# Performance work log

Measured on AMD Instinct MI355X. Metric: run time of the kernel, lower is better.

The kernel has to match this reference:

```python
import jax, jax.numpy as jnp
import numpy as np

HEAD_SIZE = 64  # hidden_size / num_attention_heads = 1024 / 16


def setup_inputs() -> dict:
    key = jax.random.key(0)
    k1, k2, k3, k4, k5 = jax.random.split(key, 5)
    B, S, H, R = 4, 2048, 1024, 1
    hidden_states = jax.random.normal(k1, (B, S, H), dtype=jnp.float32)
    attention_mask = jnp.zeros((B, S), dtype=jnp.float32)  # additive mask
    value_w = jax.random.normal(k2, (H, H), dtype=jnp.float32) * (1.0 / np.sqrt(H))
    value_b = jax.random.normal(k3, (H,), dtype=jnp.float32) * 0.02
    U = jax.random.normal(k4, (H + 1, R), dtype=jnp.float32)
    V = jax.random.normal(k5, (R, H + 1), dtype=jnp.float32)
    return {"hidden_states": hidden_states, "attention_mask": attention_mask,
            "value_w": value_w, "value_b": value_b, "U": U, "V": V}


def reference(hidden_states, attention_mask, value_w, value_b, U, V):
    B, S, H = hidden_states.shape
    # value projection (nn.Linear applies x @ W^T + b)
    value_layer = hidden_states @ value_w.T + value_b  # [B,S,H]
    # X = [hidden_states, 1] -> [B,S,H+1]
    ones = jnp.ones((B, S, 1), dtype=hidden_states.dtype)
    X = jnp.concatenate([hidden_states, ones], axis=-1)
    # scores = X (U V) X^T, computed via the low-rank factorization:
    # (X U) [B,S,R] @ (X V^T)^T [B,R,S] -- mathematically identical, avoids
    # materializing the (H+1)x(H+1) matrix M.
    XU = X @ U            # [B,S,R]
    XVt = X @ V.T         # [B,S,R]
    scores = jnp.einsum('bsr,btr->bst', XU, XVt) / jnp.sqrt(jnp.float32(HEAD_SIZE))
    # additive attention mask, broadcast as [B,1,S]
    scores = scores + attention_mask[:, None, :]
    probs = jax.nn.softmax(scores, axis=-1)  # [B,S,S]
    # dropout p=0.0 (eval) -> identity
    context = jnp.einsum('bst,bth->bsh', probs, value_layer)  # [B,S,H]
    return context
```

## Files before the change

kernel.cpp:

```cpp
#include <hip/hip_runtime.h>
#include <hip/hip_bf16.h>
#include <stdint.h>

#define LOG2E 1.44269504088896340736f

typedef float f32x4 __attribute__((ext_vector_type(4)));
typedef __bf16 bf16x8 __attribute__((ext_vector_type(8)));

__device__ __forceinline__ void g2lds16(const void* g, void* l) {
  __builtin_amdgcn_global_load_lds(
      (__attribute__((address_space(1))) unsigned int*)g,
      (__attribute__((address_space(3))) unsigned int*)l,
      16, 0, 0);
}

__device__ __forceinline__ unsigned short f2bf_u(float f) {
  __bf16 h = (__bf16)f;
  return __builtin_bit_cast(unsigned short, h);
}

__global__ void __launch_bounds__(256) fused_prep(
    const float* __restrict__ hidden, const float* __restrict__ U,
    const float* __restrict__ V, const float* __restrict__ vw,
    unsigned short* __restrict__ hbf, unsigned short* __restrict__ wbf,
    float* __restrict__ aL, float* __restrict__ vArr) {
  int tid = threadIdx.x;
  int pid = blockIdx.x;
  if (pid < 512) {
    int lane = tid & 63, w = tid >> 6;
    int xcd = pid & 7, idx = pid >> 3;
    int row0 = (xcd << 10) + (idx * 4 + w) * 4;
    float4 u4[4], v4[4];
#pragma unroll
    for (int c = 0; c < 4; ++c) {
      u4[c] = *(const float4*)&U[c * 256 + lane * 4];
      v4[c] = *(const float4*)&V[c * 256 + lane * 4];
    }
    float u_t = U[1024], v_t = V[1024];
    float su[4], sv[4];
#pragma unroll
    for (int r = 0; r < 4; ++r) {
      const float* hr = hidden + (size_t)(row0 + r) * 1024;
      unsigned short* hb = hbf + (size_t)(row0 + r) * 1024;
      float ssu = 0.f, ssv = 0.f;
#pragma unroll
      for (int c = 0; c < 4; ++c) {
        float4 x = *(const float4*)&hr[c * 256 + lane * 4];
        ushort4 o;
        o.x = f2bf_u(x.x); o.y = f2bf_u(x.y); o.z = f2bf_u(x.z); o.w = f2bf_u(x.w);
        *(ushort4*)&hb[c * 256 + lane * 4] = o;
        ssu += x.x * u4[c].x + x.y * u4[c].y + x.z * u4[c].z + x.w * u4[c].w;
        ssv += x.x * v4[c].x + x.y * v4[c].y + x.z * v4[c].z + x.w * v4[c].w;
      }
      su[r] = ssu; sv[r] = ssv;
    }
#pragma unroll
    for (int off = 1; off < 64; off <<= 1) {
#pragma unroll
      for (int r = 0; r < 4; ++r) {
        su[r] += __shfl_xor(su[r], off);
        sv[r] += __shfl_xor(sv[r], off);
      }
    }
    if (lane < 4) {
      int r = lane;
      float sur = (r == 0) ? su[0] : (r == 1) ? su[1] : (r == 2) ? su[2] : su[3];
      float svr = (r == 0) ? sv[0] : (r == 1) ? sv[1] : (r == 2) ? sv[2] : sv[3];
      aL[row0 + r] = (sur + u_t) * 0.125f * LOG2E;
      vArr[row0 + r] = svr + v_t;
    }
  } else {
    int wp = pid - 512;
#pragma unroll
    for (int it = 0; it < 8; ++it) {
      int idx = (wp * 256 + tid) * 4 + it * 131072;
      float4 x = *(const float4*)&vw[idx];
      ushort4 o;
      o.x = f2bf_u(x.x); o.y = f2bf_u(x.y); o.z = f2bf_u(x.z); o.w = f2bf_u(x.w);
      *(ushort4*)&wbf[idx] = o;
    }
  }
}

__global__ void __launch_bounds__(256) gemm_stats(
    const unsigned short* __restrict__ hbf, const unsigned short* __restrict__ wbf,
    const float* __restrict__ bias, unsigned short* __restrict__ vlt,
    const float* __restrict__ aL, const float* __restrict__ vArr,
    const float* __restrict__ mask, unsigned short* __restrict__ P,
    int statsBlocks) {
  __shared__ __align__(16) char sA[128 * 256];
  __shared__ __align__(16) char sB[128 * 256];
  int tid = threadIdx.x;
  int pid = blockIdx.x;
  if (pid >= statsBlocks) {
    int g = pid - statsBlocks;
    int lane = tid & 63, wave = tid >> 6;
    int xcd = g & 7, kk = g >> 3;
    int m0 = (xcd * 8 + (kk >> 3)) * 128;
    int n0 = (kk & 7) * 128;
    int rl = lane >> 4, pc = lane & 15;
    int wr = wave >> 1, wc = wave & 1;
    int m_ = lane & 15, q = lane >> 4;
    f32x4 acc[4][4] = {};
    for (int k0 = 0; k0 < 1024; k0 += 128) {
      __syncthreads();
#pragma unroll
      for (int ii = 0; ii < 8; ++ii) {
        int rb = wave * 32 + ii * 4;
        int r = rb + rl;
        int gc = pc ^ (r & 15);
        g2lds16(hbf + (size_t)(m0 + r) * 1024 + k0 + gc * 8, sA + rb * 256);
        g2lds16(wbf + (size_t)(n0 + r) * 1024 + k0 + gc * 8, sB + rb * 256);
      }
      __syncthreads();
#pragma unroll
      for (int ks = 0; ks < 4; ++ks) {
        bf16x8 af[4], bfr[4];
#pragma unroll
        for (int i = 0; i < 4; ++i)
          af[i] = *(const bf16x8*)(sA + (wr * 64 + i * 16 + m_) * 256 + (((ks * 4 + q) ^ m_) * 16));
#pragma unroll
        for (int j = 0; j < 4; ++j)
          bfr[j] = *(const bf16x8*)(sB + (wc * 64 + j * 16 + m_) * 256 + (((ks * 4 + q) ^ m_) * 16));
#pragma unroll
        for (int i = 0; i < 4; ++i)
#pragma unroll
          for (int j = 0; j < 4; ++j)
            acc[i][j] = __builtin_amdgcn_mfma_f32_16x16x32_bf16(af[i], bfr[j], acc[i][j], 0, 0, 0);
      }
    }
#pragma unroll
    for (int jt = 0; jt < 4; ++jt) {
      int j = n0 + wc * 64 + jt * 16 + m_;
      float bj = bias[j];
#pragma unroll
      for (int it = 0; it < 4; ++it) {
        int i = m0 + wr * 64 + it * 16 + q * 4;
        f32x4 a = acc[it][jt];
        ushort4 o;
        o.x = f2bf_u(a.x + bj); o.y = f2bf_u(a.y + bj);
        o.z = f2bf_u(a.z + bj); o.w = f2bf_u(a.w + bj);
        *(ushort4*)&vlt[(size_t)j * 8192 + i] = o;
      }
    }
  } else {
    int b = pid;
    int lane = tid & 63, w = tid >> 6;
    int xcd = b & 7, idx = b >> 3;
    int row0 = (xcd << 10) + (idx * 4 + w) * 8;
    int tb = (row0 >> 11) << 11;
    float4 va[8], ma[8];
#pragma unroll
    for (int c = 0; c < 4; ++c) {
      int t = c * 512 + lane * 8;
      va[2 * c]     = *(const float4*)&vArr[tb + t];
      va[2 * c + 1] = *(const float4*)&vArr[tb + t + 4];
      float4 m0v = *(const float4*)&mask[tb + t];
      float4 m1v = *(const float4*)&mask[tb + t + 4];
      ma[2 * c].x = m0v.x * LOG2E; ma[2 * c].y = m0v.y * LOG2E;
      ma[2 * c].z = m0v.z * LOG2E; ma[2 * c].w = m0v.w * LOG2E;
      ma[2 * c + 1].x = m1v.x * LOG2E; ma[2 * c + 1].y = m1v.y * LOG2E;
      ma[2 * c + 1].z = m1v.z * LOG2E; ma[2 * c + 1].w = m1v.w * LOG2E;
    }
#pragma unroll
    for (int r = 0; r < 8; ++r) {
      int row = row0 + r;
      float a = aL[row];
      float s[32];
#pragma unroll
      for (int qq = 0; qq < 8; ++qq) {
        s[qq * 4 + 0] = fmaf(a, va[qq].x, ma[qq].x);
        s[qq * 4 + 1] = fmaf(a, va[qq].y, ma[qq].y);
        s[qq * 4 + 2] = fmaf(a, va[qq].z, ma[qq].z);
        s[qq * 4 + 3] = fmaf(a, va[qq].w, ma[qq].w);
      }
      float mx = s[0];
#pragma unroll
      for (int u = 1; u < 32; ++u) mx = fmaxf(mx, s[u]);
#pragma unroll
      for (int off = 1; off < 64; off <<= 1) mx = fmaxf(mx, __shfl_xor(mx, off));
      float z = 0.f;
#pragma unroll
      for (int u = 0; u < 32; ++u) {
        s[u] = __builtin_amdgcn_exp2f(s[u] - mx);
        z += s[u];
      }
#pragma unroll
      for (int off = 1; off < 64; off <<= 1) z += __shfl_xor(z, off);
      float iz = __builtin_amdgcn_rcpf(z);
      unsigned short* pr = P + (size_t)row * 2048;
#pragma unroll
      for (int c = 0; c < 4; ++c) {
        bf16x8 o;
#pragma unroll
        for (int u = 0; u < 8; ++u) o[u] = (__bf16)(iz * s[c * 8 + u]);
        *(bf16x8*)&pr[c * 512 + lane * 8] = o;
      }
    }
  }
}

__global__ void __launch_bounds__(256) attn(
    const unsigned short* __restrict__ p, const unsigned short* __restrict__ vlt,
    float* __restrict__ out) {
  __shared__ __align__(16) char sA[128 * 256];
  __shared__ __align__(16) char sB[128 * 256];
  int tid = threadIdx.x;
  int lane = tid & 63, wave = tid >> 6;
  int pid = blockIdx.x;
  int xcd = pid & 7, kk = pid >> 3;
  int i0 = (xcd * 8 + (kk >> 3)) * 128;
  int h0 = (kk & 7) * 128;
  int b = i0 >> 11;
  size_t toff = (size_t)b << 11;
  int rl = lane >> 4, pc = lane & 15;
  int wr = wave >> 1, wc = wave & 1;
  int m_ = lane & 15, q = lane >> 4;
  f32x4 acc[4][4] = {};
  for (int k0 = 0; k0 < 2048; k0 += 128) {
    __syncthreads();
#pragma unroll
    for (int ii = 0; ii < 8; ++ii) {
      int rb = wave * 32 + ii * 4;
      int r = rb + rl;
      int gc = pc ^ (r & 15);
      g2lds16(p + (size_t)(i0 + r) * 2048 + k0 + gc * 8, sA + rb * 256);
      g2lds16(vlt + (size_t)(h0 + r) * 8192 + toff + k0 + gc * 8, sB + rb * 256);
    }
    __syncthreads();
#pragma unroll
    for (int ks = 0; ks < 4; ++ks) {
      bf16x8 af[4], bfr[4];
#pragma unroll
      for (int i = 0; i < 4; ++i)
        af[i] = *(const bf16x8*)(sA + (wr * 64 + i * 16 + m_) * 256 + (((ks * 4 + q) ^ m_) * 16));
#pragma unroll
      for (int j = 0; j < 4; ++j)
        bfr[j] = *(const bf16x8*)(sB + (wc * 64 + j * 16 + m_) * 256 + (((ks * 4 + q) ^ m_) * 16));
#pragma unroll
      for (int i = 0; i < 4; ++i)
#pragma unroll
        for (int j = 0; j < 4; ++j)
          acc[i][j] = __builtin_amdgcn_mfma_f32_16x16x32_bf16(af[i], bfr[j], acc[i][j], 0, 0, 0);
    }
  }
#pragma unroll
  for (int it = 0; it < 4; ++it) {
    int gi = i0 + wr * 64 + it * 16 + q * 4;
#pragma unroll
    for (int jt = 0; jt < 4; ++jt) {
      int h = h0 + wc * 64 + jt * 16 + m_;
      f32x4 a = acc[it][jt];
      out[(size_t)(gi + 0) * 1024 + h] = a.x;
      out[(size_t)(gi + 1) * 1024 + h] = a.y;
      out[(size_t)(gi + 2) * 1024 + h] = a.z;
      out[(size_t)(gi + 3) * 1024 + h] = a.w;
    }
  }
}

extern "C" void kernel_launch(void* const* d_in, const int* in_sizes, int n_in,
                              void* d_out, int out_size, void* d_ws, size_t ws_size,
                              hipStream_t stream) {
  const float* hidden = (const float*)d_in[0];
  const float* mask   = (const float*)d_in[1];
  const float* vw     = (const float*)d_in[2];
  const float* vb     = (const float*)d_in[3];
  const float* U      = (const float*)d_in[4];
  const float* V      = (const float*)d_in[5];
  float* out = (float*)d_out;
  char* ws = (char*)d_ws;

  if (ws_size >= 69271552ull) {
    unsigned short* hbf = (unsigned short*)ws;
    unsigned short* wbf = (unsigned short*)(ws + 16777216);
    unsigned short* vlt = (unsigned short*)(ws + 18874368);
    unsigned short* P   = (unsigned short*)(ws + 35651584);
    float* aL   = (float*)(ws + 69206016);
    float* vArr = aL + 8192;
    fused_prep<<<640, 256, 0, stream>>>(hidden, U, V, vw, hbf, wbf, aL, vArr);
    gemm_stats<<<768, 256, 0, stream>>>(hbf, wbf, vb, vlt, aL, vArr, mask, P, 256);
    attn<<<512, 256, 0, stream>>>(P, vlt, out);
  } else {
    unsigned short* hbf = (unsigned short*)ws;
    unsigned short* wbf = (unsigned short*)(ws + 16777216);
    unsigned short* P   = (unsigned short*)ws;
    unsigned short* vlt = (unsigned short*)(ws + 33554432);
    float* aL   = (float*)(ws + 50331648);
    float* vArr = aL + 8192;
    fused_prep<<<640, 256, 0, stream>>>(hidden, U, V, vw, hbf, wbf, aL, vArr);
    gemm_stats<<<512, 256, 0, stream>>>(hbf, wbf, vb, vlt, aL, vArr, mask, P, 0);
    gemm_stats<<<256, 256, 0, stream>>>(hbf, wbf, vb, vlt, aL, vArr, mask, P, 256);
    attn<<<512, 256, 0, stream>>>(P, vlt, out);
  }
}
```

Baseline: 157.7 us.

## Merge stats, value GEMM and attention into persistent kernel with flag-based dependencies

Replaces the separate gemm_stats and attn launches with one persistent kernel. Blocks pull work items from an atomic counter: softmax-probability rows first, then value-projection tiles, then attention output tiles. Each attention tile waits on a completion counter for P and on per-tile flags for the value tiles it needs. This removes a kernel-boundary drain and lets attention tiles start while late projection tiles finish. It adds spin-wait synchronisation, a control array reset in the prep kernel, and a risk of deadlock or stalls if dependency ordering or occupancy assumptions break.

After: 549.8 us. 3.49x slower.

```diff
diff --git a/kernel.cpp b/kernel.cpp
--- a/kernel.cpp
+++ b/kernel.cpp
@@ -23,9 +23,13 @@
     const float* __restrict__ hidden, const float* __restrict__ U,
     const float* __restrict__ V, const float* __restrict__ vw,
     unsigned short* __restrict__ hbf, unsigned short* __restrict__ wbf,
-    float* __restrict__ aL, float* __restrict__ vArr) {
+    float* __restrict__ aL, float* __restrict__ vArr,
+    unsigned int* __restrict__ ctrl) {
   int tid = threadIdx.x;
   int pid = blockIdx.x;
+  if (ctrl != nullptr && pid == 0) {
+    for (int i = tid; i < 544; i += 256) ctrl[i] = 0u;
+  }
   if (pid < 512) {
     int lane = tid & 63, w = tid >> 6;
     int xcd = pid & 7, idx = pid >> 3;
@@ -78,6 +82,203 @@
       ushort4 o;
       o.x = f2bf_u(x.x); o.y = f2bf_u(x.y); o.z = f2bf_u(x.z); o.w = f2bf_u(x.w);
       *(ushort4*)&wbf[idx] = o;
+    }
+  }
+}
+
+__global__ void __launch_bounds__(256) mega(
+    const unsigned short* __restrict__ hbf, const unsigned short* __restrict__ wbf,
+    const float* __restrict__ bias, unsigned short* __restrict__ vlt,
+    const float* __restrict__ aL, const float* __restrict__ vArr,
+    const float* __restrict__ mask, unsigned short* __restrict__ P,
+    float* __restrict__ out, unsigned int* __restrict__ ctrl) {
+  __shared__ __align__(16) char sA[128 * 256];
+  __shared__ __align__(16) char sB[128 * 256];
+  __shared__ unsigned int s_t;
+  unsigned int* flags = ctrl + 16;
+  int tid = threadIdx.x;
+  for (;;) {
+    __syncthreads();
+    if (tid == 0) s_t = atomicAdd(&ctrl[0], 1u);
+    __syncthreads();
+    unsigned int t = s_t;
+    if (t >= 1280u) return;
+    if (t < 256u) {
+      int lane = tid & 63, w = tid >> 6;
+      int row0 = (int)t * 32 + w * 8;
+      int tb = (row0 >> 11) << 11;
+      float4 va[8], ma[8];
+#pragma unroll
+      for (int c = 0; c < 4; ++c) {
+        int tt = c * 512 + lane * 8;
+        va[2 * c]     = *(const float4*)&vArr[tb + tt];
+        va[2 * c + 1] = *(const float4*)&vArr[tb + tt + 4];
+        float4 m0v = *(const float4*)&mask[tb + tt];
+        float4 m1v = *(const float4*)&mask[tb + tt + 4];
+        ma[2 * c].x = m0v.x * LOG2E; ma[2 * c].y = m0v.y * LOG2E;
+        ma[2 * c].z = m0v.z * LOG2E; ma[2 * c].w = m0v.w * LOG2E;
+        ma[2 * c + 1].x = m1v.x * LOG2E; ma[2 * c + 1].y = m1v.y * LOG2E;
+        ma[2 * c + 1].z = m1v.z * LOG2E; ma[2 * c + 1].w = m1v.w * LOG2E;
+      }
+#pragma unroll
+      for (int r = 0; r < 8; ++r) {
+        int row = row0 + r;
+        float a = aL[row];
+        float s[32];
+#pragma unroll
+        for (int qq = 0; qq < 8; ++qq) {
+          s[qq * 4 + 0] = fmaf(a, va[qq].x, ma[qq].x);
+          s[qq * 4 + 1] = fmaf(a, va[qq].y, ma[qq].y);
+          s[qq * 4 + 2] = fmaf(a, va[qq].z, ma[qq].z);
+          s[qq * 4 + 3] = fmaf(a, va[qq].w, ma[qq].w);
+        }
+        float mx = s[0];
+#pragma unroll
+        for (int u = 1; u < 32; ++u) mx = fmaxf(mx, s[u]);
+#pragma unroll
+        for (int off = 1; off < 64; off <<= 1) mx = fmaxf(mx, __shfl_xor(mx, off));
+        float z = 0.f;
+#pragma unroll
+        for (int u = 0; u < 32; ++u) {
+          s[u] = __builtin_amdgcn_exp2f(s[u] - mx);
+          z += s[u];
+        }
+#pragma unroll
+        for (int off = 1; off < 64; off <<= 1) z += __shfl_xor(z, off);
+        float iz = __builtin_amdgcn_rcpf(z);
+        unsigned short* pr = P + (size_t)row * 2048;
+#pragma unroll
+        for (int c = 0; c < 4; ++c) {
+          bf16x8 o;
+#pragma unroll
+          for (int u = 0; u < 8; ++u) o[u] = (__bf16)(iz * s[c * 8 + u]);
+          *(bf16x8*)&pr[c * 512 + lane * 8] = o;
+        }
+      }
+      __syncthreads();
+      if (tid == 0) {
+        __threadfence();
+        __hip_atomic_fetch_add(&ctrl[1], 1u, __ATOMIC_RELEASE, __HIP_MEMORY_SCOPE_AGENT);
+      }
+    } else if (t < 768u) {
+      unsigned int fq = t - 256u;
+      int m0 = (int)(fq & 63u) * 128;
+      int n0 = (int)(fq >> 6) * 128;
+      int lane = tid & 63, wave = tid >> 6;
+      int rl = lane >> 4, pc = lane & 15;
+      int wr = wave >> 1, wc = wave & 1;
+      int m_ = lane & 15, qq = lane >> 4;
+      f32x4 acc[4][4] = {};
+      for (int k0 = 0; k0 < 1024; k0 += 128) {
+        __syncthreads();
+#pragma unroll
+        for (int ii = 0; ii < 8; ++ii) {
+          int rb = wave * 32 + ii * 4;
+          int r = rb + rl;
+          int gc = pc ^ (r & 15);
+          g2lds16(hbf + (size_t)(m0 + r) * 1024 + k0 + gc * 8, sA + rb * 256);
+          g2lds16(wbf + (size_t)(n0 + r) * 1024 + k0 + gc * 8, sB + rb * 256);
+        }
+        __syncthreads();
+#pragma unroll
+        for (int ks = 0; ks < 4; ++ks) {
+          bf16x8 af[4], bfr[4];
+#pragma unroll
+          for (int i = 0; i < 4; ++i)
+            af[i] = *(const bf16x8*)(sA + (wr * 64 + i * 16 + m_) * 256 + (((ks * 4 + qq) ^ m_) * 16));
+#pragma unroll
+          for (int j = 0; j < 4; ++j)
+            bfr[j] = *(const bf16x8*)(sB + (wc * 64 + j * 16 + m_) * 256 + (((ks * 4 + qq) ^ m_) * 16));
+#pragma unroll
+          for (int i = 0; i < 4; ++i)
+#pragma unroll
+            for (int j = 0; j < 4; ++j)
+              acc[i][j] = __builtin_amdgcn_mfma_f32_16x16x32_bf16(af[i], bfr[j], acc[i][j], 0, 0, 0);
+        }
+      }
+#pragma unroll
+      for (int jt = 0; jt < 4; ++jt) {
+        int j = n0 + wc * 64 + jt * 16 + m_;
+        float bj = bias[j];
+#pragma unroll
+        for (int it = 0; it < 4; ++it) {
+          int i = m0 + wr * 64 + it * 16 + qq * 4;
+          f32x4 a = acc[it][jt];
+          ushort4 o;
+          o.x = f2bf_u(a.x + bj); o.y = f2bf_u(a.y + bj);
+          o.z = f2bf_u(a.z + bj); o.w = f2bf_u(a.w + bj);
+          *(ushort4*)&vlt[(size_t)j * 8192 + i] = o;
+        }
+      }
+      __syncthreads();
+      if (tid == 0) {
+        __threadfence();
+        __hip_atomic_store(&flags[fq], 1u, __ATOMIC_RELEASE, __HIP_MEMORY_SCOPE_AGENT);
+      }
+    } else {
+      unsigned int at = t - 768u;
+      int N = (int)(at >> 6), I = (int)(at & 63u);
+      int i0 = I * 128, h0 = N * 128;
+      int b = I >> 4;
+      size_t toff = (size_t)b << 11;
+      unsigned int qbase = ((unsigned)N << 6) | ((unsigned)b << 4);
+      int lane = tid & 63, wave = tid >> 6;
+      int rl = lane >> 4, pc = lane & 15;
+      int wr = wave >> 1, wc = wave & 1;
+      int m_ = lane & 15, qq = lane >> 4;
+      if (tid == 0) {
+        while (__hip_atomic_load(&ctrl[1], __ATOMIC_ACQUIRE, __HIP_MEMORY_SCOPE_AGENT) < 256u)
+          __builtin_amdgcn_s_sleep(2);
+        __threadfence();
+      }
+      f32x4 acc[4][4] = {};
+      for (int k0 = 0; k0 < 2048; k0 += 128) {
+        __syncthreads();
+        if (tid == 0) {
+          unsigned int fq = qbase + (unsigned)(k0 >> 7);
+          while (__hip_atomic_load(&flags[fq], __ATOMIC_ACQUIRE, __HIP_MEMORY_SCOPE_AGENT) == 0u)
+            __builtin_amdgcn_s_sleep(2);
+          __threadfence();
+        }
+        __syncthreads();
+#pragma unroll
+        for (int ii = 0; ii < 8; ++ii) {
+          int rb = wave * 32 + ii * 4;
+          int r = rb + rl;
+          int gc = pc ^ (r & 15);
+          g2lds16(P + (size_t)(i0 + r) * 2048 + k0 + gc * 8, sA + rb * 256);
+          g2lds16(vlt + (size_t)(h0 + r) * 8192 + toff + k0 + gc * 8, sB + rb * 256);
+        }
+        __syncthreads();
+#pragma unroll
+        for (int ks = 0; ks < 4; ++ks) {
+          bf16x8 af[4], bfr[4];
+#pragma unroll
+          for (int i = 0; i < 4; ++i)
+            af[i] = *(const bf16x8*)(sA + (wr * 64 + i * 16 + m_) * 256 + (((ks * 4 + qq) ^ m_) * 16));
+#pragma unroll
+          for (int j = 0; j < 4; ++j)
+            bfr[j] = *(const bf16x8*)(sB + (wc * 64 + j * 16 + m_) * 256 + (((ks * 4 + qq) ^ m_) * 16));
+#pragma unroll
+          for (int i = 0; i < 4; ++i)
+#pragma unroll
+            for (int j = 0; j < 4; ++j)
+              acc[i][j] = __builtin_amdgcn_mfma_f32_16x16x32_bf16(af[i], bfr[j], acc[i][j], 0, 0, 0);
+        }
+      }
+#pragma unroll
+      for (int it = 0; it < 4; ++it) {
+        int gi = i0 + wr * 64 + it * 16 + qq * 4;
+#pragma unroll
+        for (int jt = 0; jt < 4; ++jt) {
+          int h = h0 + wc * 64 + jt * 16 + m_;
+          f32x4 a = acc[it][jt];
+          out[(size_t)(gi + 0) * 1024 + h] = a.x;
+          out[(size_t)(gi + 1) * 1024 + h] = a.y;
+          out[(size_t)(gi + 2) * 1024 + h] = a.z;
+          out[(size_t)(gi + 3) * 1024 + h] = a.w;
+        }
+      }
     }
   }
 }
@@ -271,16 +472,16 @@
   float* out = (float*)d_out;
   char* ws = (char*)d_ws;
 
-  if (ws_size >= 69271552ull) {
+  if (ws_size >= 69275648ull) {
     unsigned short* hbf = (unsigned short*)ws;
     unsigned short* wbf = (unsigned short*)(ws + 16777216);
     unsigned short* vlt = (unsigned short*)(ws + 18874368);
     unsigned short* P   = (unsigned short*)(ws + 35651584);
     float* aL   = (float*)(ws + 69206016);
     float* vArr = aL + 8192;
-    fused_prep<<<640, 256, 0, stream>>>(hidden, U, V, vw, hbf, wbf, aL, vArr);
-    gemm_stats<<<768, 256, 0, stream>>>(hbf, wbf, vb, vlt, aL, vArr, mask, P, 256);
-    attn<<<512, 256, 0, stream>>>(P, vlt, out);
+    unsigned int* ctrl = (unsigned int*)(ws + 69271552);
+    fused_prep<<<640, 256, 0, stream>>>(hidden, U, V, vw, hbf, wbf, aL, vArr, ctrl);
+    mega<<<512, 256, 0, stream>>>(hbf, wbf, vb, vlt, aL, vArr, mask, P, out, ctrl);
   } else {
     unsigned short* hbf = (unsigned short*)ws;
     unsigned short* wbf = (unsigned short*)(ws + 16777216);
@@ -288,7 +489,7 @@
     unsigned short* vlt = (unsigned short*)(ws + 33554432);
     float* aL   = (float*)(ws + 50331648);
     float* vArr = aL + 8192;
-    fused_prep<<<640, 256, 0, stream>>>(hidden, U, V, vw, hbf, wbf, aL, vArr);
+    fused_prep<<<640, 256, 0, stream>>>(hidden, U, V, vw, hbf, wbf, aL, vArr, nullptr);
     gemm_stats<<<512, 256, 0, stream>>>(hbf, wbf, vb, vlt, aL, vArr, mask, P, 0);
     gemm_stats<<<256, 256, 0, stream>>>(hbf, wbf, vb, vlt, aL, vArr, mask, P, 256);
     attn<<<512, 256, 0, stream>>>(P, vlt, out);
```

## Double-buffer LDS tiles with async prefetch in value GEMM and attention GEMM

Applied to the files above, without the earlier changes.

Both bf16 GEMM loops move from a single 128-wide K tile loaded and then computed under two full syncthreads to two 64-wide K buffers. The next tile is prefetched with global_load_lds while the current one is computed, using an explicit vmcnt wait and raw s_barrier. The goal is to hide global-to-LDS load latency behind MFMA work. In exchange, the K step is halved, doubling the number of barriers, and the swizzle changes to an 8-chunk XOR pattern. The hand-written vmcnt counts depend on the exact number of outstanding loads per thread.

After: 166.1 us. +5.3%, slower.

```diff
diff --git a/kernel.cpp b/kernel.cpp
--- a/kernel.cpp
+++ b/kernel.cpp
@@ -88,8 +88,8 @@
     const float* __restrict__ aL, const float* __restrict__ vArr,
     const float* __restrict__ mask, unsigned short* __restrict__ P,
     int statsBlocks) {
-  __shared__ __align__(16) char sA[128 * 256];
-  __shared__ __align__(16) char sB[128 * 256];
+  __shared__ __align__(16) char sA[2][128 * 128];
+  __shared__ __align__(16) char sB[2][128 * 128];
   int tid = threadIdx.x;
   int pid = blockIdx.x;
   if (pid >= statsBlocks) {
@@ -98,36 +98,55 @@
     int xcd = g & 7, kk = g >> 3;
     int m0 = (xcd * 8 + (kk >> 3)) * 128;
     int n0 = (kk & 7) * 128;
-    int rl = lane >> 4, pc = lane & 15;
+    int r8 = lane >> 3, c8 = lane & 7;
     int wr = wave >> 1, wc = wave & 1;
     int m_ = lane & 15, q = lane >> 4;
+#pragma unroll
+    for (int ii = 0; ii < 4; ++ii) {
+      int rb = wave * 32 + ii * 8;
+      int r = rb + r8;
+      int gc = c8 ^ (r & 7);
+      g2lds16(hbf + (size_t)(m0 + r) * 1024 + gc * 8, sA[0] + rb * 128);
+      g2lds16(wbf + (size_t)(n0 + r) * 1024 + gc * 8, sB[0] + rb * 128);
+    }
     f32x4 acc[4][4] = {};
-    for (int k0 = 0; k0 < 1024; k0 += 128) {
-      __syncthreads();
-#pragma unroll
-      for (int ii = 0; ii < 8; ++ii) {
-        int rb = wave * 32 + ii * 4;
-        int r = rb + rl;
-        int gc = pc ^ (r & 15);
-        g2lds16(hbf + (size_t)(m0 + r) * 1024 + k0 + gc * 8, sA + rb * 256);
-        g2lds16(wbf + (size_t)(n0 + r) * 1024 + k0 + gc * 8, sB + rb * 256);
-      }
-      __syncthreads();
-#pragma unroll
-      for (int ks = 0; ks < 4; ++ks) {
+    for (int k = 0; k < 16; ++k) {
+      int cur = k & 1;
+      if (k < 15) {
+        int k0n = (k + 1) * 64;
+#pragma unroll
+        for (int ii = 0; ii < 4; ++ii) {
+          int rb = wave * 32 + ii * 8;
+          int r = rb + r8;
+          int gc = c8 ^ (r & 7);
+          g2lds16(hbf + (size_t)(m0 + r) * 1024 + k0n + gc * 8, sA[cur ^ 1] + rb * 128);
+          g2lds16(wbf + (size_t)(n0 + r) * 1024 + k0n + gc * 8, sB[cur ^ 1] + rb * 128);
+        }
+        asm volatile("s_waitcnt vmcnt(8)" ::: "memory");
+      } else {
+        asm volatile("s_waitcnt vmcnt(0)" ::: "memory");
+      }
+      __builtin_amdgcn_s_barrier();
+      asm volatile("" ::: "memory");
+      const char* ca = sA[cur];
+      const char* cb = sB[cur];
+#pragma unroll
+      for (int ks = 0; ks < 2; ++ks) {
         bf16x8 af[4], bfr[4];
 #pragma unroll
         for (int i = 0; i < 4; ++i)
-          af[i] = *(const bf16x8*)(sA + (wr * 64 + i * 16 + m_) * 256 + (((ks * 4 + q) ^ m_) * 16));
+          af[i] = *(const bf16x8*)(ca + (wr * 64 + i * 16 + m_) * 128 + (((ks * 4 + q) ^ (m_ & 7)) * 16));
 #pragma unroll
         for (int j = 0; j < 4; ++j)
-          bfr[j] = *(const bf16x8*)(sB + (wc * 64 + j * 16 + m_) * 256 + (((ks * 4 + q) ^ m_) * 16));
+          bfr[j] = *(const bf16x8*)(cb + (wc * 64 + j * 16 + m_) * 128 + (((ks * 4 + q) ^ (m_ & 7)) * 16));
 #pragma unroll
         for (int i = 0; i < 4; ++i)
 #pragma unroll
           for (int j = 0; j < 4; ++j)
             acc[i][j] = __builtin_amdgcn_mfma_f32_16x16x32_bf16(af[i], bfr[j], acc[i][j], 0, 0, 0);
       }
+      asm volatile("" ::: "memory");
+      __builtin_amdgcn_s_barrier();
     }
 #pragma unroll
     for (int jt = 0; jt < 4; ++jt) {
@@ -203,8 +222,8 @@
 __global__ void __launch_bounds__(256) attn(
     const unsigned short* __restrict__ p, const unsigned short* __restrict__ vlt,
     float* __restrict__ out) {
-  __shared__ __align__(16) char sA[128 * 256];
-  __shared__ __align__(16) char sB[128 * 256];
+  __shared__ __align__(16) char sA[2][128 * 128];
+  __shared__ __align__(16) char sB[2][128 * 128];
   int tid = threadIdx.x;
   int lane = tid & 63, wave = tid >> 6;
   int pid = blockIdx.x;
@@ -213,36 +232,55 @@
   int h0 = (kk & 7) * 128;
   int b = i0 >> 11;
   size_t toff = (size_t)b << 11;
-  int rl = lane >> 4, pc = lane & 15;
+  int r8 = lane >> 3, c8 = lane & 7;
   int wr = wave >> 1, wc = wave & 1;
   int m_ = lane & 15, q = lane >> 4;
+#pragma unroll
+  for (int ii = 0; ii < 4; ++ii) {
+    int rb = wave * 32 + ii * 8;
+    int r = rb + r8;
+    int gc = c8 ^ (r & 7);
+    g2lds16(p + (size_t)(i0 + r) * 2048 + gc * 8, sA[0] + rb * 128);
+    g2lds16(vlt + (size_t)(h0 + r) * 8192 + toff + gc * 8, sB[0] + rb * 128);
+  }
   f32x4 acc[4][4] = {};
-  for (int k0 = 0; k0 < 2048; k0 += 128) {
-    __syncthreads();
-#pragma unroll
-    for (int ii = 0; ii < 8; ++ii) {
-      int rb = wave * 32 + ii * 4;
-      int r = rb + rl;
-      int gc = pc ^ (r & 15);
-      g2lds16(p + (size_t)(i0 + r) * 2048 + k0 + gc * 8, sA + rb * 256);
-      g2lds16(vlt + (size_t)(h0 + r) * 8192 + toff + k0 + gc * 8, sB + rb * 256);
-    }
-    __syncthreads();
-#pragma unroll
-    for (int ks = 0; ks < 4; ++ks) {
+  for (int k = 0; k < 32; ++k) {
+    int cur = k & 1;
+    if (k < 31) {
+      int k0n = (k + 1) * 64;
+#pragma unroll
+      for (int ii = 0; ii < 4; ++ii) {
+        int rb = wave * 32 + ii * 8;
+        int r = rb + r8;
+        int gc = c8 ^ (r & 7);
+        g2lds16(p + (size_t)(i0 + r) * 2048 + k0n + gc * 8, sA[cur ^ 1] + rb * 128);
+        g2lds16(vlt + (size_t)(h0 + r) * 8192 + toff + k0n + gc * 8, sB[cur ^ 1] + rb * 128);
+      }
+      asm volatile("s_waitcnt vmcnt(8)" ::: "memory");
+    } else {
+      asm volatile("s_waitcnt vmcnt(0)" ::: "memory");
+    }
+    __builtin_amdgcn_s_barrier();
+    asm volatile("" ::: "memory");
+    const char* ca = sA[cur];
+    const char* cb = sB[cur];
+#pragma unroll
+    for (int ks = 0; ks < 2; ++ks) {
       bf16x8 af[4], bfr[4];
 #pragma unroll
       for (int i = 0; i < 4; ++i)
-        af[i] = *(const bf16x8*)(sA + (wr * 64 + i * 16 + m_) * 256 + (((ks * 4 + q) ^ m_) * 16));
+        af[i] = *(const bf16x8*)(ca + (wr * 64 + i * 16 + m_) * 128 + (((ks * 4 + q) ^ (m_ & 7)) * 16));
 #pragma unroll
       for (int j = 0; j < 4; ++j)
-        bfr[j] = *(const bf16x8*)(sB + (wc * 64 + j * 16 + m_) * 256 + (((ks * 4 + q) ^ m_) * 16));
+        bfr[j] = *(const bf16x8*)(cb + (wc * 64 + j * 16 + m_) * 128 + (((ks * 4 + q) ^ (m_ & 7)) * 16));
 #pragma unroll
       for (int i = 0; i < 4; ++i)
 #pragma unroll
         for (int j = 0; j < 4; ++j)
           acc[i][j] = __builtin_amdgcn_mfma_f32_16x16x32_bf16(af[i], bfr[j], acc[i][j], 0, 0, 0);
     }
+    asm volatile("" ::: "memory");
+    __builtin_amdgcn_s_barrier();
   }
 #pragma unroll
   for (int it = 0; it < 4; ++it) {
```

## Triple-buffer attn PV GEMM with 256x128 tiles and 512-thread blocks

Applied to the files above, without the earlier changes.

Rewrites the final probs×V GEMM kernel to use 256x128 output tiles computed by 8 waves, with a 3-stage LDS ring of 64-wide K slices loaded asynchronously. Explicit vmcnt waits and one barrier per step replace the two-barrier load/compute pattern, and s_setprio is raised around the MFMA blocks. The aim is to overlap global→LDS traffic with MFMA work and to reload the B tile less often. In exchange it uses more LDS (about 144KB) and more accumulator registers per wave, and launches only 256 blocks, which may limit occupancy on the CUs.

Result: slower. 172.4 us (+9.4%).

```diff
diff --git a/kernel.cpp b/kernel.cpp
--- a/kernel.cpp
+++ b/kernel.cpp
@@ -200,57 +200,91 @@
   }
 }
 
-__global__ void __launch_bounds__(256) attn(
-    const unsigned short* __restrict__ p, const unsigned short* __restrict__ vlt,
+__global__ void __launch_bounds__(512, 2) attn(
+    const unsigned short* __restrict__ P, const unsigned short* __restrict__ vlt,
     float* __restrict__ out) {
-  __shared__ __align__(16) char sA[128 * 256];
-  __shared__ __align__(16) char sB[128 * 256];
+  __shared__ __align__(16) char sA[3][256 * 128];
+  __shared__ __align__(16) char sB[3][128 * 128];
   int tid = threadIdx.x;
   int lane = tid & 63, wave = tid >> 6;
   int pid = blockIdx.x;
   int xcd = pid & 7, kk = pid >> 3;
-  int i0 = (xcd * 8 + (kk >> 3)) * 128;
+  int mt = xcd * 4 + (kk >> 3);
+  int i0 = mt * 256;
   int h0 = (kk & 7) * 128;
-  int b = i0 >> 11;
-  size_t toff = (size_t)b << 11;
-  int rl = lane >> 4, pc = lane & 15;
-  int wr = wave >> 1, wc = wave & 1;
+  size_t toff = (size_t)(mt >> 3) << 11;
+  int r8 = lane >> 3, c8 = lane & 7;
+  int wr = wave >> 2, wcn = wave & 3;
   int m_ = lane & 15, q = lane >> 4;
-  f32x4 acc[4][4] = {};
-  for (int k0 = 0; k0 < 2048; k0 += 128) {
-    __syncthreads();
-#pragma unroll
-    for (int ii = 0; ii < 8; ++ii) {
-      int rb = wave * 32 + ii * 4;
-      int r = rb + rl;
-      int gc = pc ^ (r & 15);
-      g2lds16(p + (size_t)(i0 + r) * 2048 + k0 + gc * 8, sA + rb * 256);
-      g2lds16(vlt + (size_t)(h0 + r) * 8192 + toff + k0 + gc * 8, sB + rb * 256);
-    }
-    __syncthreads();
-#pragma unroll
-    for (int ks = 0; ks < 4; ++ks) {
-      bf16x8 af[4], bfr[4];
-#pragma unroll
-      for (int i = 0; i < 4; ++i)
-        af[i] = *(const bf16x8*)(sA + (wr * 64 + i * 16 + m_) * 256 + (((ks * 4 + q) ^ m_) * 16));
-#pragma unroll
-      for (int j = 0; j < 4; ++j)
-        bfr[j] = *(const bf16x8*)(sB + (wc * 64 + j * 16 + m_) * 256 + (((ks * 4 + q) ^ m_) * 16));
-#pragma unroll
-      for (int i = 0; i < 4; ++i)
-#pragma unroll
-        for (int j = 0; j < 4; ++j)
-          acc[i][j] = __builtin_amdgcn_mfma_f32_16x16x32_bf16(af[i], bfr[j], acc[i][j], 0, 0, 0);
-    }
-  }
-#pragma unroll
-  for (int it = 0; it < 4; ++it) {
-    int gi = i0 + wr * 64 + it * 16 + q * 4;
-#pragma unroll
-    for (int jt = 0; jt < 4; ++jt) {
-      int h = h0 + wc * 64 + jt * 16 + m_;
-      f32x4 a = acc[it][jt];
+
+#define ATTN_STAGE(kt, ab)                                                     \
+  do {                                                                         \
+    int k0_ = (kt) * 64;                                                       \
+    _Pragma("unroll") for (int ii = 0; ii < 4; ++ii) {                         \
+      int rb = wave * 32 + ii * 8;                                             \
+      int r = rb + r8;                                                         \
+      int gc = c8 ^ (r & 7);                                                   \
+      g2lds16(P + (size_t)(i0 + r) * 2048 + k0_ + gc * 8, sA[ab] + rb * 128);  \
+    }                                                                          \
+    _Pragma("unroll") for (int ii = 0; ii < 2; ++ii) {                         \
+      int rb = wave * 16 + ii * 8;                                             \
+      int r = rb + r8;                                                         \
+      int gc = c8 ^ (r & 7);                                                   \
+      g2lds16(vlt + (size_t)(h0 + r) * 8192 + toff + k0_ + gc * 8,             \
+              sB[ab] + rb * 128);                                              \
+    }                                                                          \
+  } while (0)
+
+  ATTN_STAGE(0, 0);
+  ATTN_STAGE(1, 1);
+  asm volatile("s_waitcnt vmcnt(6)" ::: "memory");
+  __builtin_amdgcn_s_barrier();
+  asm volatile("" ::: "memory");
+
+  f32x4 acc[8][2] = {};
+  int bc = 0, bs = 2;
+  for (int t = 0; t < 32; ++t) {
+    if (t < 30) ATTN_STAGE(t + 2, bs);
+    const char* ca = sA[bc];
+    const char* cb = sB[bc];
+#pragma unroll
+    for (int ks = 0; ks < 2; ++ks) {
+      bf16x8 af[8], bfr[2];
+#pragma unroll
+      for (int m = 0; m < 8; ++m)
+        af[m] = *(const bf16x8*)(ca + (wr * 128 + m * 16 + m_) * 128 +
+                                 (((ks * 4 + q) ^ (m_ & 7)) * 16));
+#pragma unroll
+      for (int n = 0; n < 2; ++n)
+        bfr[n] = *(const bf16x8*)(cb + (wcn * 32 + n * 16 + m_) * 128 +
+                                  (((ks * 4 + q) ^ (m_ & 7)) * 16));
+      __builtin_amdgcn_s_setprio(1);
+#pragma unroll
+      for (int m = 0; m < 8; ++m)
+#pragma unroll
+        for (int n = 0; n < 2; ++n)
+          acc[m][n] = __builtin_amdgcn_mfma_f32_16x16x32_bf16(af[m], bfr[n],
+                                                              acc[m][n], 0, 0, 0);
+      __builtin_amdgcn_s_setprio(0);
+    }
+    if (t < 30)
+      asm volatile("s_waitcnt vmcnt(6)" ::: "memory");
+    else
+      asm volatile("s_waitcnt vmcnt(0)" ::: "memory");
+    __builtin_amdgcn_s_barrier();
+    asm volatile("" ::: "memory");
+    bc = (bc == 2) ? 0 : bc + 1;
+    bs = (bs == 2) ? 0 : bs + 1;
+  }
+#undef ATTN_STAGE
+
+#pragma unroll
+  for (int m = 0; m < 8; ++m) {
+    int gi = i0 + wr * 128 + m * 16 + q * 4;
+#pragma unroll
+    for (int n = 0; n < 2; ++n) {
+      int h = h0 + wcn * 32 + n * 16 + m_;
+      f32x4 a = acc[m][n];
       out[(size_t)(gi + 0) * 1024 + h] = a.x;
       out[(size_t)(gi + 1) * 1024 + h] = a.y;
       out[(size_t)(gi + 2) * 1024 + h] = a.z;
@@ -280,7 +314,7 @@
     float* vArr = aL + 8192;
     fused_prep<<<640, 256, 0, stream>>>(hidden, U, V, vw, hbf, wbf, aL, vArr);
     gemm_stats<<<768, 256, 0, stream>>>(hbf, wbf, vb, vlt, aL, vArr, mask, P, 256);
-    attn<<<512, 256, 0, stream>>>(P, vlt, out);
+    attn<<<256, 512, 0, stream>>>(P, vlt, out);
   } else {
     unsigned short* hbf = (unsigned short*)ws;
     unsigned short* wbf = (unsigned short*)(ws + 16777216);
@@ -291,6 +325,6 @@
     fused_prep<<<640, 256, 0, stream>>>(hidden, U, V, vw, hbf, wbf, aL, vArr);
     gemm_stats<<<512, 256, 0, stream>>>(hbf, wbf, vb, vlt, aL, vArr, mask, P, 0);
     gemm_stats<<<256, 256, 0, stream>>>(hbf, wbf, vb, vlt, aL, vArr, mask, P, 256);
-    attn<<<512, 256, 0, stream>>>(P, vlt, out);
-  }
-}
+    attn<<<256, 512, 0, stream>>>(P, vlt, out);
+  }
+}
```
